# Kernel tuning notes

Measured on AMD Instinct MI355X. Metric: run time of the kernel, lower is better.

Reference implementation:

```python
import jax, jax.numpy as jnp
import numpy as np

N = 100000      # nodes
E = 1600000     # edges
F = 92          # raw node feature length
H = 128         # element_embedding == hidden_encoding (GatedGraphConv out_channels)
STEPS = 6       # mpnn_steps
G = 256         # graphs in batch


def setup_inputs() -> dict:
    key = jax.random.key(0)
    ks = jax.random.split(key, 10)
    s = 0.05
    x = jax.random.normal(ks[0], (N, F), dtype=jnp.float32)
    edge_index = jax.random.randint(ks[1], (2, E), 0, N, dtype=jnp.int64)
    batch = jnp.sort(jax.random.randint(ks[2], (N,), 0, G, dtype=jnp.int64))
    # atom_input: Linear(F, H, bias=False); applied as x @ W_embed with W_embed [F, H]
    W_embed = jax.random.normal(ks[3], (F, H), dtype=jnp.float32) * s
    # GatedGraphConv weight: [num_layers, H, H], used as h @ W_mpnn[i]
    W_mpnn = jax.random.normal(ks[4], (STEPS, H, H), dtype=jnp.float32) * s
    # torch.nn.GRUCell params: weight_ih/hh [3H, H], bias_ih/hh [3H]
    w_ih = jax.random.normal(ks[5], (3 * H, H), dtype=jnp.float32) * s
    w_hh = jax.random.normal(ks[6], (3 * H, H), dtype=jnp.float32) * s
    b_ih = jax.random.normal(ks[7], (3 * H,), dtype=jnp.float32) * s
    b_hh = jax.random.normal(ks[8], (3 * H,), dtype=jnp.float32) * s
    # prediction_layer: Linear(H, 1)
    w_pred = jax.random.normal(ks[9], (H, 1), dtype=jnp.float32) * s
    b_pred = jnp.zeros((1,), dtype=jnp.float32)
    return {"x": x, "edge_index": edge_index, "batch": batch,
            "W_embed": W_embed, "W_mpnn": W_mpnn,
            "w_ih": w_ih, "w_hh": w_hh, "b_ih": b_ih, "b_hh": b_hh,
            "w_pred": w_pred, "b_pred": b_pred}


def reference(x, edge_index, batch, W_embed, W_mpnn, w_ih, w_hh, b_ih, b_hh, w_pred, b_pred):
    n = x.shape[0]
    src, dst = edge_index[0], edge_index[1]  # PyG: messages flow source -> target
    # atom_input (no bias) + tanh; element_embedding == H so no zero-padding needed
    h = jnp.tanh(x @ W_embed)  # [N, H]

    def step(h, W):
        m = h @ W                                             # per-step linear [N, H]
        agg = jax.ops.segment_sum(m[src], dst, num_segments=n)  # scatter-add aggr
        # torch GRUCell(input=agg, hidden=h)
        gi = agg @ w_ih.T + b_ih                              # [N, 3H]
        gh = h @ w_hh.T + b_hh                                # [N, 3H]
        i_r, i_z, i_n = jnp.split(gi, 3, axis=-1)
        h_r, h_z, h_n = jnp.split(gh, 3, axis=-1)
        r = jax.nn.sigmoid(i_r + h_r)
        z = jax.nn.sigmoid(i_z + h_z)
        cand = jnp.tanh(i_n + r * h_n)
        h_new = (1.0 - z) * cand + z * h
        return h_new, None

    h, _ = jax.lax.scan(step, h, W_mpnn)

    # global_mean_pool over graph ids
    sums = jax.ops.segment_sum(h, batch, num_segments=G)                           # [G, H]
    counts = jax.ops.segment_sum(jnp.ones((n, 1), h.dtype), batch, num_segments=G)  # [G, 1]
    pooled = sums / jnp.maximum(counts, 1.0)
    pooled = jax.nn.relu(pooled)
    return (pooled @ w_pred + b_pred)[:, 0]  # [G]
```

## Files before the change

### kernel.cpp

```cpp
#include <hip/hip_runtime.h>
#include <math.h>

#define N_NODES 100000
#define N_PAD   100032
#define N_EDGES 1600000
#define F_IN    92
#define H_DIM   128
#define STEPS   6
#define G_GRAPHS 256
#define TH3     384
#define SSTR    136
#define HSTR    132
#define FPASS   8
#define FRANGE  12500

typedef __attribute__((ext_vector_type(8))) short bf16x8;
typedef __attribute__((ext_vector_type(4))) float f32x4;

__device__ __forceinline__ unsigned short f2bf(float x) {
    unsigned u = __float_as_uint(x);
    return (unsigned short)((u + 0x7fffu + ((u >> 16) & 1u)) >> 16);
}
__device__ __forceinline__ float bf2f(unsigned short h) {
    return __uint_as_float(((unsigned)h) << 16);
}

__global__ void fuse_w_kernel(const float* __restrict__ Wm, const float* __restrict__ w_ih,
                              float* __restrict__ M2) {
    int ij = blockIdx.x;
    int i  = ij / TH3;
    int j  = ij - i * TH3;
    int k  = threadIdx.x;
    __shared__ float wj[H_DIM];
    wj[k] = w_ih[j * H_DIM + k];
    __syncthreads();
    const float* wr = Wm + ((size_t)i * H_DIM + k) * H_DIM;
    float acc = 0.f;
    #pragma unroll 4
    for (int c = 0; c < H_DIM; ++c) acc = fmaf(wj[c], wr[c], acc);
    M2[((size_t)i * TH3 + j) * H_DIM + k] = acc;
}

__global__ void pack_kernel(const float* __restrict__ M6, const float* __restrict__ w_hh,
                            unsigned short* __restrict__ PBhi, unsigned short* __restrict__ PBlo) {
    int b    = blockIdx.x;
    int lane = threadIdx.x;
    int kc   = b & 3;
    int ct   = (b >> 2) & 7;
    int mg   = b >> 5;
    int g    = mg % 3;
    int mat  = mg / 3;
    int j    = g * 128 + ct * 16 + (lane & 15);
    int k0   = kc * 32 + (lane >> 4) * 8;
    size_t outBase = ((size_t)b * 64 + lane) * 8;
    #pragma unroll
    for (int jj = 0; jj < 8; ++jj) {
        int k = k0 + jj;
        float v = (mat < 6) ? M6[((size_t)mat * TH3 + j) * H_DIM + k]
                            : w_hh[(size_t)j * H_DIM + k];
        unsigned short hv = f2bf(v);
        PBhi[outBase + jj] = hv;
        PBlo[outBase + jj] = f2bf(v - bf2f(hv));
    }
}

#define ET 16
__global__ void embed_kernel(const float* __restrict__ x, const float* __restrict__ We,
                             unsigned short* __restrict__ h_hi, unsigned short* __restrict__ h_lo) {
    int n0 = blockIdx.x * ET;
    int j  = threadIdx.x;
    __shared__ float xs[ET * F_IN];
    for (int i = j; i < ET * F_IN; i += H_DIM) xs[i] = x[n0 * F_IN + i];
    __syncthreads();
    float acc[ET];
    #pragma unroll
    for (int n = 0; n < ET; ++n) acc[n] = 0.f;
    const float4* xs4 = (const float4*)xs;
    for (int k4 = 0; k4 < F_IN / 4; ++k4) {
        int k = k4 * 4;
        float w0 = We[(k + 0) * H_DIM + j];
        float w1 = We[(k + 1) * H_DIM + j];
        float w2 = We[(k + 2) * H_DIM + j];
        float w3 = We[(k + 3) * H_DIM + j];
        #pragma unroll
        for (int n = 0; n < ET; ++n) {
            float4 a = xs4[n * (F_IN / 4) + k4];
            acc[n] = fmaf(a.x, w0, acc[n]);
            acc[n] = fmaf(a.y, w1, acc[n]);
            acc[n] = fmaf(a.z, w2, acc[n]);
            acc[n] = fmaf(a.w, w3, acc[n]);
        }
    }
    #pragma unroll
    for (int n = 0; n < ET; ++n) {
        float e2 = __expf(2.f * acc[n]);
        float v  = 1.f - 2.f / (e2 + 1.f);
        size_t o = (size_t)(n0 + n) * H_DIM + j;
        unsigned short hv = f2bf(v);
        h_hi[o] = hv;
        h_lo[o] = f2bf(v - bf2f(hv));
    }
}

__global__ void hist_kernel(const int* __restrict__ dst, int* __restrict__ count) {
    int e = blockIdx.x * 256 + threadIdx.x;
    if (e < N_EDGES) atomicAdd(&count[dst[e]], 1);
}

__global__ void scan_block_kernel(const int* __restrict__ count, int* __restrict__ offs,
                                  int* __restrict__ blockSums) {
    __shared__ int tmp[256];
    int i = blockIdx.x * 256 + threadIdx.x;
    int t = threadIdx.x;
    int v = (i < N_NODES) ? count[i] : 0;
    tmp[t] = v;
    __syncthreads();
    for (int d = 1; d < 256; d <<= 1) {
        int add = (t >= d) ? tmp[t - d] : 0;
        __syncthreads();
        tmp[t] += add;
        __syncthreads();
    }
    if (i < N_NODES) offs[i] = tmp[t] - v;
    if (t == 255) blockSums[blockIdx.x] = tmp[255];
}

__global__ void scan_sums_kernel(int* __restrict__ blockSums, int nb) {
    __shared__ int tmp[512];
    int t = threadIdx.x;
    int v = (t < nb) ? blockSums[t] : 0;
    tmp[t] = v;
    __syncthreads();
    for (int d = 1; d < 512; d <<= 1) {
        int add = (t >= d) ? tmp[t - d] : 0;
        __syncthreads();
        tmp[t] += add;
        __syncthreads();
    }
    if (t < nb) blockSums[t] = tmp[t] - v;
}

__global__ void scan_add_kernel(int* __restrict__ offs, const int* __restrict__ blockSums) {
    int i = blockIdx.x * 256 + threadIdx.x;
    if (i < N_NODES) offs[i] += blockSums[blockIdx.x];
    if (i == 0) offs[N_NODES] = N_EDGES;
}

__global__ void fill_kernel(const int* __restrict__ src, const int* __restrict__ dst,
                            const int* __restrict__ offs, int* __restrict__ cursor,
                            int* __restrict__ srcSorted) {
    int e = blockIdx.x * 256 + threadIdx.x;
    if (e >= N_EDGES) return;
    for (int p = 0; p < FPASS; ++p) {
        int lo = p * FRANGE;
        int d = dst[e];
        if (d >= lo && d < lo + FRANGE) {
            int pos = atomicAdd(&cursor[d], 1);
            srcSorted[offs[d] + pos] = src[e];
        }
    }
}

__global__ void gather_kernel(const unsigned short* __restrict__ h_hi,
                              const int* __restrict__ offs, const int* __restrict__ srcS,
                              unsigned short* __restrict__ sv) {
    int tid  = blockIdx.x * 256 + threadIdx.x;
    int node = tid >> 4;
    int c8   = (tid & 15) * 8;
    float a[8];
    #pragma unroll
    for (int j = 0; j < 8; ++j) a[j] = 0.f;
    if (node < N_NODES) {
        int beg = offs[node], end = offs[node + 1];
        int i = beg;
        for (; i + 4 <= end; i += 4) {
            int n0 = srcS[i], n1 = srcS[i + 1], n2 = srcS[i + 2], n3 = srcS[i + 3];
            bf16x8 v0 = *(const bf16x8*)(h_hi + (size_t)n0 * H_DIM + c8);
            bf16x8 v1 = *(const bf16x8*)(h_hi + (size_t)n1 * H_DIM + c8);
            bf16x8 v2 = *(const bf16x8*)(h_hi + (size_t)n2 * H_DIM + c8);
            bf16x8 v3 = *(const bf16x8*)(h_hi + (size_t)n3 * H_DIM + c8);
            #pragma unroll
            for (int j = 0; j < 8; ++j)
                a[j] += (bf2f((unsigned short)v0[j]) + bf2f((unsigned short)v1[j]))
                      + (bf2f((unsigned short)v2[j]) + bf2f((unsigned short)v3[j]));
        }
        if (i + 2 <= end) {
            int n0 = srcS[i], n1 = srcS[i + 1];
            bf16x8 v0 = *(const bf16x8*)(h_hi + (size_t)n0 * H_DIM + c8);
            bf16x8 v1 = *(const bf16x8*)(h_hi + (size_t)n1 * H_DIM + c8);
            #pragma unroll
            for (int j = 0; j < 8; ++j)
                a[j] += bf2f((unsigned short)v0[j]) + bf2f((unsigned short)v1[j]);
            i += 2;
        }
        if (i < end) {
            int n0 = srcS[i];
            bf16x8 v0 = *(const bf16x8*)(h_hi + (size_t)n0 * H_DIM + c8);
            #pragma unroll
            for (int j = 0; j < 8; ++j) a[j] += bf2f((unsigned short)v0[j]);
        }
    }
    bf16x8 o;
    #pragma unroll
    for (int j = 0; j < 8; ++j) o[j] = (short)f2bf(a[j]);
    *(bf16x8*)(sv + (size_t)node * H_DIM + c8) = o;
}

__global__ __launch_bounds__(512, 4) void gru_kernel(
    const unsigned short* __restrict__ sv,
    unsigned short* __restrict__ h_hi, unsigned short* __restrict__ h_lo,
    const unsigned short* __restrict__ PBhi, const unsigned short* __restrict__ PBlo,
    int matI, const float* __restrict__ b_ih, const float* __restrict__ b_hh)
{
    __shared__ __align__(16) unsigned short buf[2 * 32 * SSTR];
    unsigned short* sHh = buf;
    unsigned short* sHl = buf + 32 * SSTR;
    float* hnF = (float*)buf;

    int nt = blockIdx.x;
    int rowBase = nt * 32;
    int t = threadIdx.x;

    {
        int row = t >> 4;
        int c8  = (t & 15) * 8;
        size_t g = (size_t)(rowBase + row) * H_DIM + c8;
        int l = row * SSTR + c8;
        *(bf16x8*)&sHh[l] = *(const bf16x8*)(h_hi + g);
        *(bf16x8*)&sHl[l] = *(const bf16x8*)(h_lo + g);
    }
    __syncthreads();

    int lane = t & 63;
    int ct   = t >> 6;
    int rloc = lane & 15;
    int kOff = (lane >> 4) * 8;

    f32x4 accRZ[2][2], accIn[2], accHn[2];
    #pragma unroll
    for (int rs = 0; rs < 2; ++rs) {
        accRZ[0][rs] = (f32x4){0.f, 0.f, 0.f, 0.f};
        accRZ[1][rs] = (f32x4){0.f, 0.f, 0.f, 0.f};
        accIn[rs]    = (f32x4){0.f, 0.f, 0.f, 0.f};
        accHn[rs]    = (f32x4){0.f, 0.f, 0.f, 0.f};
    }

    const int fI0 = matI * 3;
    for (int kc = 0; kc < 4; ++kc) {
        int aOff = kc * 32 + kOff;
        bf16x8 aS[2];
        #pragma unroll
        for (int rs = 0; rs < 2; ++rs)
            aS[rs] = *(const bf16x8*)(sv + (size_t)(rowBase + rs * 16 + rloc) * H_DIM + aOff);
        bf16x8 aHh4[2], aHl4[2];
        #pragma unroll
        for (int rs = 0; rs < 2; ++rs) {
            int al = (rs * 16 + rloc) * SSTR + aOff;
            aHh4[rs] = *(const bf16x8*)(&sHh[al]);
            aHl4[rs] = *(const bf16x8*)(&sHl[al]);
        }
        #pragma unroll
        for (int g = 0; g < 3; ++g) {
            size_t oI = ((size_t)((fI0 + g) * 32 + ct * 4 + kc) * 64 + lane) * 8;
            size_t oH = ((size_t)((18  + g) * 32 + ct * 4 + kc) * 64 + lane) * 8;
            bf16x8 bIh = *(const bf16x8*)(PBhi + oI);
            bf16x8 bIl = *(const bf16x8*)(PBlo + oI);
            bf16x8 bHh = *(const bf16x8*)(PBhi + oH);
            bf16x8 bHl = *(const bf16x8*)(PBlo + oH);
            #pragma unroll
            for (int rs = 0; rs < 2; ++rs) {
                f32x4* tI = (g == 0) ? &accRZ[0][rs] : (g == 1) ? &accRZ[1][rs] : &accIn[rs];
                f32x4* tH = (g == 2) ? &accHn[rs] : tI;
                *tI = __builtin_amdgcn_mfma_f32_16x16x32_bf16(aS[rs],   bIh, *tI, 0, 0, 0);
                *tI = __builtin_amdgcn_mfma_f32_16x16x32_bf16(aS[rs],   bIl, *tI, 0, 0, 0);
                *tH = __builtin_amdgcn_mfma_f32_16x16x32_bf16(aHh4[rs], bHh, *tH, 0, 0, 0);
                *tH = __builtin_amdgcn_mfma_f32_16x16x32_bf16(aHl4[rs], bHh, *tH, 0, 0, 0);
                *tH = __builtin_amdgcn_mfma_f32_16x16x32_bf16(aHh4[rs], bHl, *tH, 0, 0, 0);
            }
        }
    }

    int c = ct * 16 + rloc;
    float br  = b_ih[c] + b_hh[c];
    float bz  = b_ih[128 + c] + b_hh[128 + c];
    float bin = b_ih[256 + c], bhn = b_hh[256 + c];
    int rl = (lane >> 4) * 4;

    float hnv[2][4];
    #pragma unroll
    for (int rs = 0; rs < 2; ++rs) {
        #pragma unroll
        for (int r = 0; r < 4; ++r) {
            int lrow = rs * 16 + rl + r;
            float hold = bf2f(sHh[lrow * SSTR + c]) + bf2f(sHl[lrow * SSTR + c]);
            float rr = 1.f / (1.f + __expf(-(accRZ[0][rs][r] + br)));
            float zz = 1.f / (1.f + __expf(-(accRZ[1][rs][r] + bz)));
            float pre = (accIn[rs][r] + bin) + rr * (accHn[rs][r] + bhn);
            float e2 = __expf(2.f * pre);
            float cand = 1.f - 2.f / (e2 + 1.f);
            hnv[rs][r] = (1.f - zz) * cand + zz * hold;
        }
    }
    __syncthreads();
    #pragma unroll
    for (int rs = 0; rs < 2; ++rs)
        #pragma unroll
        for (int r = 0; r < 4; ++r)
            hnF[(rs * 16 + rl + r) * HSTR + c] = hnv[rs][r];
    __syncthreads();
    #pragma unroll
    for (int i = t; i < 32 * 32; i += 512) {
        int row = i >> 5;
        int c4  = (i & 31) * 4;
        int gRow = rowBase + row;
        if (gRow < N_NODES) {
            float4 v = *(const float4*)(&hnF[row * HSTR + c4]);
            ushort4 hh, ll;
            hh.x = f2bf(v.x); ll.x = f2bf(v.x - bf2f(hh.x));
            hh.y = f2bf(v.y); ll.y = f2bf(v.y - bf2f(hh.y));
            hh.z = f2bf(v.z); ll.z = f2bf(v.z - bf2f(hh.z));
            hh.w = f2bf(v.w); ll.w = f2bf(v.w - bf2f(hh.w));
            size_t o = (size_t)gRow * H_DIM + c4;
            *(ushort4*)(h_hi + o) = hh;
            *(ushort4*)(h_lo + o) = ll;
        }
    }
}

__global__ void pool_partial(const unsigned short* __restrict__ h_hi,
                             const unsigned short* __restrict__ h_lo,
                             const int* __restrict__ batch,
                             float* __restrict__ pooled) {
    int b = blockIdx.x;
    int t = threadIdx.x;
    int n0 = b * 64;
    if (n0 >= N_NODES) return;
    int nEnd = n0 + 64 < N_NODES ? n0 + 64 : N_NODES;
    int curG = batch[n0];
    float acc = 0.f;
    for (int n = n0; n < nEnd; ++n) {
        int g = batch[n];
        if (g != curG) {
            atomicAdd(&pooled[curG * H_DIM + t], acc);
            acc = 0.f;
            curG = g;
        }
        size_t o = (size_t)n * H_DIM + t;
        acc += bf2f(h_hi[o]) + bf2f(h_lo[o]);
    }
    atomicAdd(&pooled[curG * H_DIM + t], acc);
}

__global__ void pool_head(const float* __restrict__ pooled, const int* __restrict__ batch,
                          const float* __restrict__ w_pred, const float* __restrict__ b_pred,
                          float* __restrict__ out) {
    int g = blockIdx.x;
    int t = threadIdx.x;
    __shared__ int bounds[2];
    __shared__ float red[2];
    if (t < 2) {
        int target = g + t;
        int lo = 0, hi = N_NODES;
        while (lo < hi) {
            int mid = (lo + hi) >> 1;
            if (batch[mid] < target) lo = mid + 1; else hi = mid;
        }
        bounds[t] = lo;
    }
    __syncthreads();
    int cnt = bounds[1] - bounds[0];
    float pv = pooled[g * H_DIM + t] / fmaxf((float)cnt, 1.f);
    pv = fmaxf(pv, 0.f);
    float v = pv * w_pred[t];
    #pragma unroll
    for (int off = 32; off > 0; off >>= 1) v += __shfl_down(v, off);
    if ((t & 63) == 0) red[t >> 6] = v;
    __syncthreads();
    if (t == 0) out[g] = red[0] + red[1] + b_pred[0];
}

extern "C" void kernel_launch(void* const* d_in, const int* in_sizes, int n_in,
                              void* d_out, int out_size, void* d_ws, size_t ws_size,
                              hipStream_t stream) {
    const float* x      = (const float*)d_in[0];
    const int*   ei     = (const int*)d_in[1];
    const int*   batch  = (const int*)d_in[2];
    const float* We     = (const float*)d_in[3];
    const float* Wm     = (const float*)d_in[4];
    const float* w_ih   = (const float*)d_in[5];
    const float* w_hh   = (const float*)d_in[6];
    const float* b_ih   = (const float*)d_in[7];
    const float* b_hh   = (const float*)d_in[8];
    const float* w_pred = (const float*)d_in[9];
    const float* b_pred = (const float*)d_in[10];
    float* out = (float*)d_out;

    const size_t HN = (size_t)N_PAD * H_DIM;
    unsigned short* h_hi = (unsigned short*)d_ws;
    unsigned short* h_lo = h_hi + HN;
    unsigned short* sv   = h_lo + HN;
    float* M6 = (float*)(sv + HN);
    unsigned short* PBhi = (unsigned short*)(M6 + (size_t)STEPS * TH3 * H_DIM);
    unsigned short* PBlo = PBhi + 21 * 32 * 64 * 8;
    int* offs      = (int*)(PBlo + 21 * 32 * 64 * 8);
    int* srcSorted = offs + (N_NODES + 1);
    float* pooled  = (float*)(srcSorted + N_EDGES);
    int* count     = (int*)sv;
    int* cursor    = count + N_NODES;
    int* blockSums = cursor + N_NODES;

    const int* esrc = ei;
    const int* edst = ei + N_EDGES;
    const int EB = (N_EDGES + 255) / 256;
    const int NB = (N_NODES + 255) / 256;

    hipMemsetAsync(count, 0, 2 * (size_t)N_NODES * sizeof(int), stream);
    hipMemsetAsync(pooled, 0, (size_t)G_GRAPHS * H_DIM * sizeof(float), stream);
    hist_kernel<<<EB, 256, 0, stream>>>(edst, count);
    scan_block_kernel<<<NB, 256, 0, stream>>>(count, offs, blockSums);
    scan_sums_kernel<<<1, 512, 0, stream>>>(blockSums, NB);
    scan_add_kernel<<<NB, 256, 0, stream>>>(offs, blockSums);
    fill_kernel<<<EB, 256, 0, stream>>>(esrc, edst, offs, cursor, srcSorted);

    fuse_w_kernel<<<STEPS * TH3, H_DIM, 0, stream>>>(Wm, w_ih, M6);
    pack_kernel<<<21 * 32, 64, 0, stream>>>(M6, w_hh, PBhi, PBlo);
    embed_kernel<<<N_NODES / ET, H_DIM, 0, stream>>>(x, We, h_hi, h_lo);

    for (int i = 0; i < STEPS; ++i) {
        gather_kernel<<<(N_PAD * 16) / 256, 256, 0, stream>>>(h_hi, offs, srcSorted, sv);
        gru_kernel<<<N_PAD / 32, 512, 0, stream>>>(sv, h_hi, h_lo, PBhi, PBlo,
                                                   i, b_ih, b_hh);
    }

    pool_partial<<<(N_NODES + 63) / 64, H_DIM, 0, stream>>>(h_hi, h_lo, batch, pooled);
    pool_head<<<G_GRAPHS, H_DIM, 0, stream>>>(pooled, batch, w_pred, b_pred, out);
}
```

Measured before the change: 1.175 ms.

## Fuse neighbor gather into GRU kernel with ping-pong hidden buffers

Moves the edge aggregation into the GRU kernel. Each block gathers its 32 nodes' neighbor sums into shared memory, which removes the separate gather launch and the global round trip of the aggregated tensor. The hidden-state hi part is now double-buffered so that blocks reading neighbors never see rows already updated. The hidden-side MFMAs are issued before the synchronisation so they can overlap with gather latency. The cost is extra shared memory per block, which may lower occupancy, and the gather now runs under the GRU kernel's launch configuration.

```diff
diff --git a/kernel.cpp b/kernel.cpp
--- a/kernel.cpp
+++ b/kernel.cpp
@@ -161,75 +161,74 @@
     }
 }
 
-__global__ void gather_kernel(const unsigned short* __restrict__ h_hi,
-                              const int* __restrict__ offs, const int* __restrict__ srcS,
-                              unsigned short* __restrict__ sv) {
-    int tid  = blockIdx.x * 256 + threadIdx.x;
-    int node = tid >> 4;
-    int c8   = (tid & 15) * 8;
-    float a[8];
-    #pragma unroll
-    for (int j = 0; j < 8; ++j) a[j] = 0.f;
-    if (node < N_NODES) {
-        int beg = offs[node], end = offs[node + 1];
-        int i = beg;
-        for (; i + 4 <= end; i += 4) {
-            int n0 = srcS[i], n1 = srcS[i + 1], n2 = srcS[i + 2], n3 = srcS[i + 3];
-            bf16x8 v0 = *(const bf16x8*)(h_hi + (size_t)n0 * H_DIM + c8);
-            bf16x8 v1 = *(const bf16x8*)(h_hi + (size_t)n1 * H_DIM + c8);
-            bf16x8 v2 = *(const bf16x8*)(h_hi + (size_t)n2 * H_DIM + c8);
-            bf16x8 v3 = *(const bf16x8*)(h_hi + (size_t)n3 * H_DIM + c8);
-            #pragma unroll
-            for (int j = 0; j < 8; ++j)
-                a[j] += (bf2f((unsigned short)v0[j]) + bf2f((unsigned short)v1[j]))
-                      + (bf2f((unsigned short)v2[j]) + bf2f((unsigned short)v3[j]));
-        }
-        if (i + 2 <= end) {
-            int n0 = srcS[i], n1 = srcS[i + 1];
-            bf16x8 v0 = *(const bf16x8*)(h_hi + (size_t)n0 * H_DIM + c8);
-            bf16x8 v1 = *(const bf16x8*)(h_hi + (size_t)n1 * H_DIM + c8);
-            #pragma unroll
-            for (int j = 0; j < 8; ++j)
-                a[j] += bf2f((unsigned short)v0[j]) + bf2f((unsigned short)v1[j]);
-            i += 2;
-        }
-        if (i < end) {
-            int n0 = srcS[i];
-            bf16x8 v0 = *(const bf16x8*)(h_hi + (size_t)n0 * H_DIM + c8);
-            #pragma unroll
-            for (int j = 0; j < 8; ++j) a[j] += bf2f((unsigned short)v0[j]);
-        }
-    }
-    bf16x8 o;
-    #pragma unroll
-    for (int j = 0; j < 8; ++j) o[j] = (short)f2bf(a[j]);
-    *(bf16x8*)(sv + (size_t)node * H_DIM + c8) = o;
-}
-
-__global__ __launch_bounds__(512, 4) void gru_kernel(
-    const unsigned short* __restrict__ sv,
-    unsigned short* __restrict__ h_hi, unsigned short* __restrict__ h_lo,
+__global__ __launch_bounds__(512, 4) void gru_fused_kernel(
+    const unsigned short* __restrict__ h_hi_in,
+    unsigned short* __restrict__ h_hi_out,
+    unsigned short* __restrict__ h_lo,
+    const int* __restrict__ offs, const int* __restrict__ srcS,
     const unsigned short* __restrict__ PBhi, const unsigned short* __restrict__ PBlo,
     int matI, const float* __restrict__ b_ih, const float* __restrict__ b_hh)
 {
-    __shared__ __align__(16) unsigned short buf[2 * 32 * SSTR];
+    __shared__ __align__(16) unsigned short buf[3 * 32 * SSTR];
     unsigned short* sHh = buf;
     unsigned short* sHl = buf + 32 * SSTR;
+    unsigned short* sS  = buf + 2 * 32 * SSTR;
     float* hnF = (float*)buf;
 
     int nt = blockIdx.x;
     int rowBase = nt * 32;
     int t = threadIdx.x;
+    int row = t >> 4;
+    int c8  = (t & 15) * 8;
 
     {
-        int row = t >> 4;
-        int c8  = (t & 15) * 8;
         size_t g = (size_t)(rowBase + row) * H_DIM + c8;
         int l = row * SSTR + c8;
-        *(bf16x8*)&sHh[l] = *(const bf16x8*)(h_hi + g);
+        *(bf16x8*)&sHh[l] = *(const bf16x8*)(h_hi_in + g);
         *(bf16x8*)&sHl[l] = *(const bf16x8*)(h_lo + g);
     }
     __syncthreads();
+
+    {
+        float a[8];
+        #pragma unroll
+        for (int j = 0; j < 8; ++j) a[j] = 0.f;
+        int node = rowBase + row;
+        if (node < N_NODES) {
+            int beg = offs[node], end = offs[node + 1];
+            int i = beg;
+            for (; i + 4 <= end; i += 4) {
+                int n0 = srcS[i], n1 = srcS[i + 1], n2 = srcS[i + 2], n3 = srcS[i + 3];
+                bf16x8 v0 = *(const bf16x8*)(h_hi_in + (size_t)n0 * H_DIM + c8);
+                bf16x8 v1 = *(const bf16x8*)(h_hi_in + (size_t)n1 * H_DIM + c8);
+                bf16x8 v2 = *(const bf16x8*)(h_hi_in + (size_t)n2 * H_DIM + c8);
+                bf16x8 v3 = *(const bf16x8*)(h_hi_in + (size_t)n3 * H_DIM + c8);
+                #pragma unroll
+                for (int j = 0; j < 8; ++j)
+                    a[j] += (bf2f((unsigned short)v0[j]) + bf2f((unsigned short)v1[j]))
+                          + (bf2f((unsigned short)v2[j]) + bf2f((unsigned short)v3[j]));
+            }
+            if (i + 2 <= end) {
+                int n0 = srcS[i], n1 = srcS[i + 1];
+                bf16x8 v0 = *(const bf16x8*)(h_hi_in + (size_t)n0 * H_DIM + c8);
+                bf16x8 v1 = *(const bf16x8*)(h_hi_in + (size_t)n1 * H_DIM + c8);
+                #pragma unroll
+                for (int j = 0; j < 8; ++j)
+                    a[j] += bf2f((unsigned short)v0[j]) + bf2f((unsigned short)v1[j]);
+                i += 2;
+            }
+            if (i < end) {
+                int n0 = srcS[i];
+                bf16x8 v0 = *(const bf16x8*)(h_hi_in + (size_t)n0 * H_DIM + c8);
+                #pragma unroll
+                for (int j = 0; j < 8; ++j) a[j] += bf2f((unsigned short)v0[j]);
+            }
+        }
+        bf16x8 o;
+        #pragma unroll
+        for (int j = 0; j < 8; ++j) o[j] = (short)f2bf(a[j]);
+        *(bf16x8*)&sS[row * SSTR + c8] = o;
+    }
 
     int lane = t & 63;
     int ct   = t >> 6;
@@ -245,37 +244,49 @@
         accHn[rs]    = (f32x4){0.f, 0.f, 0.f, 0.f};
     }
 
+    for (int kc = 0; kc < 4; ++kc) {
+        int aOff = kc * 32 + kOff;
+        bf16x8 aHh4[2], aHl4[2];
+        #pragma unroll
+        for (int rs = 0; rs < 2; ++rs) {
+            int al = (rs * 16 + rloc) * SSTR + aOff;
+            aHh4[rs] = *(const bf16x8*)(&sHh[al]);
+            aHl4[rs] = *(const bf16x8*)(&sHl[al]);
+        }
+        #pragma unroll
+        for (int g = 0; g < 3; ++g) {
+            size_t oH = ((size_t)((18 + g) * 32 + ct * 4 + kc) * 64 + lane) * 8;
+            bf16x8 bHh = *(const bf16x8*)(PBhi + oH);
+            bf16x8 bHl = *(const bf16x8*)(PBlo + oH);
+            #pragma unroll
+            for (int rs = 0; rs < 2; ++rs) {
+                f32x4* tH = (g == 0) ? &accRZ[0][rs] : (g == 1) ? &accRZ[1][rs] : &accHn[rs];
+                *tH = __builtin_amdgcn_mfma_f32_16x16x32_bf16(aHh4[rs], bHh, *tH, 0, 0, 0);
+                *tH = __builtin_amdgcn_mfma_f32_16x16x32_bf16(aHl4[rs], bHh, *tH, 0, 0, 0);
+                *tH = __builtin_amdgcn_mfma_f32_16x16x32_bf16(aHh4[rs], bHl, *tH, 0, 0, 0);
+            }
+        }
+    }
+
+    __syncthreads();
+
     const int fI0 = matI * 3;
     for (int kc = 0; kc < 4; ++kc) {
         int aOff = kc * 32 + kOff;
         bf16x8 aS[2];
         #pragma unroll
         for (int rs = 0; rs < 2; ++rs)
-            aS[rs] = *(const bf16x8*)(sv + (size_t)(rowBase + rs * 16 + rloc) * H_DIM + aOff);
-        bf16x8 aHh4[2], aHl4[2];
-        #pragma unroll
-        for (int rs = 0; rs < 2; ++rs) {
-            int al = (rs * 16 + rloc) * SSTR + aOff;
-            aHh4[rs] = *(const bf16x8*)(&sHh[al]);
-            aHl4[rs] = *(const bf16x8*)(&sHl[al]);
-        }
+            aS[rs] = *(const bf16x8*)(&sS[(rs * 16 + rloc) * SSTR + aOff]);
         #pragma unroll
         for (int g = 0; g < 3; ++g) {
             size_t oI = ((size_t)((fI0 + g) * 32 + ct * 4 + kc) * 64 + lane) * 8;
-            size_t oH = ((size_t)((18  + g) * 32 + ct * 4 + kc) * 64 + lane) * 8;
             bf16x8 bIh = *(const bf16x8*)(PBhi + oI);
             bf16x8 bIl = *(const bf16x8*)(PBlo + oI);
-            bf16x8 bHh = *(const bf16x8*)(PBhi + oH);
-            bf16x8 bHl = *(const bf16x8*)(PBlo + oH);
             #pragma unroll
             for (int rs = 0; rs < 2; ++rs) {
                 f32x4* tI = (g == 0) ? &accRZ[0][rs] : (g == 1) ? &accRZ[1][rs] : &accIn[rs];
-                f32x4* tH = (g == 2) ? &accHn[rs] : tI;
-                *tI = __builtin_amdgcn_mfma_f32_16x16x32_bf16(aS[rs],   bIh, *tI, 0, 0, 0);
-                *tI = __builtin_amdgcn_mfma_f32_16x16x32_bf16(aS[rs],   bIl, *tI, 0, 0, 0);
-                *tH = __builtin_amdgcn_mfma_f32_16x16x32_bf16(aHh4[rs], bHh, *tH, 0, 0, 0);
-                *tH = __builtin_amdgcn_mfma_f32_16x16x32_bf16(aHl4[rs], bHh, *tH, 0, 0, 0);
-                *tH = __builtin_amdgcn_mfma_f32_16x16x32_bf16(aHh4[rs], bHl, *tH, 0, 0, 0);
+                *tI = __builtin_amdgcn_mfma_f32_16x16x32_bf16(aS[rs], bIh, *tI, 0, 0, 0);
+                *tI = __builtin_amdgcn_mfma_f32_16x16x32_bf16(aS[rs], bIl, *tI, 0, 0, 0);
             }
         }
     }
@@ -310,18 +321,18 @@
     __syncthreads();
     #pragma unroll
     for (int i = t; i < 32 * 32; i += 512) {
-        int row = i >> 5;
-        int c4  = (i & 31) * 4;
-        int gRow = rowBase + row;
+        int rw = i >> 5;
+        int c4 = (i & 31) * 4;
+        int gRow = rowBase + rw;
         if (gRow < N_NODES) {
-            float4 v = *(const float4*)(&hnF[row * HSTR + c4]);
+            float4 v = *(const float4*)(&hnF[rw * HSTR + c4]);
             ushort4 hh, ll;
             hh.x = f2bf(v.x); ll.x = f2bf(v.x - bf2f(hh.x));
             hh.y = f2bf(v.y); ll.y = f2bf(v.y - bf2f(hh.y));
             hh.z = f2bf(v.z); ll.z = f2bf(v.z - bf2f(hh.z));
             hh.w = f2bf(v.w); ll.w = f2bf(v.w - bf2f(hh.w));
             size_t o = (size_t)gRow * H_DIM + c4;
-            *(ushort4*)(h_hi + o) = hh;
+            *(ushort4*)(h_hi_out + o) = hh;
             *(ushort4*)(h_lo + o) = ll;
         }
     }
@@ -396,16 +407,16 @@
     float* out = (float*)d_out;
 
     const size_t HN = (size_t)N_PAD * H_DIM;
-    unsigned short* h_hi = (unsigned short*)d_ws;
-    unsigned short* h_lo = h_hi + HN;
-    unsigned short* sv   = h_lo + HN;
-    float* M6 = (float*)(sv + HN);
+    unsigned short* h_hiA = (unsigned short*)d_ws;
+    unsigned short* h_lo  = h_hiA + HN;
+    unsigned short* h_hiB = h_lo + HN;
+    float* M6 = (float*)(h_hiB + HN);
     unsigned short* PBhi = (unsigned short*)(M6 + (size_t)STEPS * TH3 * H_DIM);
     unsigned short* PBlo = PBhi + 21 * 32 * 64 * 8;
     int* offs      = (int*)(PBlo + 21 * 32 * 64 * 8);
     int* srcSorted = offs + (N_NODES + 1);
     float* pooled  = (float*)(srcSorted + N_EDGES);
-    int* count     = (int*)sv;
+    int* count     = (int*)h_hiB;
     int* cursor    = count + N_NODES;
     int* blockSums = cursor + N_NODES;
 
@@ -424,14 +435,16 @@
 
     fuse_w_kernel<<<STEPS * TH3, H_DIM, 0, stream>>>(Wm, w_ih, M6);
     pack_kernel<<<21 * 32, 64, 0, stream>>>(M6, w_hh, PBhi, PBlo);
-    embed_kernel<<<N_NODES / ET, H_DIM, 0, stream>>>(x, We, h_hi, h_lo);
+    embed_kernel<<<N_NODES / ET, H_DIM, 0, stream>>>(x, We, h_hiA, h_lo);
 
     for (int i = 0; i < STEPS; ++i) {
-        gather_kernel<<<(N_PAD * 16) / 256, 256, 0, stream>>>(h_hi, offs, srcSorted, sv);
-        gru_kernel<<<N_PAD / 32, 512, 0, stream>>>(sv, h_hi, h_lo, PBhi, PBlo,
-                                                   i, b_ih, b_hh);
-    }
-
-    pool_partial<<<(N_NODES + 63) / 64, H_DIM, 0, stream>>>(h_hi, h_lo, batch, pooled);
+        const unsigned short* hin = (i & 1) ? h_hiB : h_hiA;
+        unsigned short*       hout = (i & 1) ? h_hiA : h_hiB;
+        gru_fused_kernel<<<N_PAD / 32, 512, 0, stream>>>(hin, hout, h_lo,
+                                                         offs, srcSorted, PBhi, PBlo,
+                                                         i, b_ih, b_hh);
+    }
+
+    pool_partial<<<(N_NODES + 63) / 64, H_DIM, 0, stream>>>(h_hiA, h_lo, batch, pooled);
     pool_head<<<G_GRAPHS, H_DIM, 0, stream>>>(pooled, batch, w_pred, b_pred, out);
 }
```

After: 1.107 ms. 1.06x faster.
